# Kernel tuning notes

Hardware: AMD Instinct MI355X
Metric: run time of the kernel (lower is better)

The kernel has to match this reference:

```python
import jax, jax.numpy as jnp
import numpy as np

EPS = 1e-5


def ternarize(w):
    # TWN: delta = 0.7*mean|w|; alpha = mean of |w| over entries above delta
    delta = 0.7 * jnp.mean(jnp.abs(w))
    mask = (jnp.abs(w) > delta).astype(w.dtype)
    alpha = jnp.sum(jnp.abs(w) * mask) / jnp.maximum(jnp.sum(mask), 1.0)
    q = alpha * jnp.sign(w) * mask
    # straight-through estimator (matches torch `w + (q - w).detach()`)
    return w + jax.lax.stop_gradient(q - w)


def conv2d(x, w, stride, pad):
    # x: NCHW, w: OIHW
    return jax.lax.conv_general_dilated(
        x, w, window_strides=(stride, stride), padding=[(pad, pad), (pad, pad)],
        dimension_numbers=("NCHW", "OIHW", "NCHW"))


def batchnorm(x, gamma, beta, mean, var):
    # inference-mode BN over channel dim of NCHW
    inv = gamma / jnp.sqrt(var + EPS)
    return x * inv[None, :, None, None] + (beta - mean * inv)[None, :, None, None]


def setup_inputs() -> dict:
    key = jax.random.key(0)
    ks = jax.random.split(key, 12)
    d = {
        "x": jax.random.normal(ks[0], (64, 3, 224, 224), jnp.float32),
        "w1": jax.random.normal(ks[1], (32, 3, 3, 3), jnp.float32) * 0.1,
        "g1": jnp.ones((32,), jnp.float32), "b1": jnp.zeros((32,), jnp.float32),
        "m1": jax.random.normal(ks[2], (32,), jnp.float32) * 0.1,
        "v1": jax.random.uniform(ks[3], (32,), jnp.float32, 0.5, 1.5),
        "w2": jax.random.normal(ks[4], (64, 32, 3, 3), jnp.float32) * 0.05,
        "g2": jnp.ones((64,), jnp.float32), "b2": jnp.zeros((64,), jnp.float32),
        "m2": jax.random.normal(ks[5], (64,), jnp.float32) * 0.1,
        "v2": jax.random.uniform(ks[6], (64,), jnp.float32, 0.5, 1.5),
        "w3": jax.random.normal(ks[7], (128, 64, 3, 3), jnp.float32) * 0.05,
        "g3": jnp.ones((128,), jnp.float32), "b3": jnp.zeros((128,), jnp.float32),
        "m3": jax.random.normal(ks[8], (128,), jnp.float32) * 0.1,
        "v3": jax.random.uniform(ks[9], (128,), jnp.float32, 0.5, 1.5),
        "wl": jax.random.normal(ks[10], (10, 128), jnp.float32) * 0.1,
        "bl": jax.random.normal(ks[11], (10,), jnp.float32) * 0.01,
    }
    return d


def reference(x, w1, g1, b1, m1, v1, w2, g2, b2, m2, v2,
              w3, g3, b3, m3, v3, wl, bl):
    h = jax.nn.relu(batchnorm(conv2d(x, ternarize(w1), 2, 1), g1, b1, m1, v1))
    h = jax.nn.relu(batchnorm(conv2d(h, ternarize(w2), 1, 1), g2, b2, m2, v2))
    h = jax.nn.relu(batchnorm(conv2d(h, ternarize(w3), 2, 1), g3, b3, m3, v3))
    h = jnp.mean(h, axis=(2, 3))  # AdaptiveAvgPool2d((1,1)) + flatten -> [N,128]
    return h @ ternarize(wl).T + bl
```

## Files before the change

kernel.cpp:

```cpp
#include <hip/hip_runtime.h>
#include <cstddef>

typedef __attribute__((ext_vector_type(8))) short short8;
typedef __attribute__((ext_vector_type(4))) float floatx4;

__device__ __forceinline__ unsigned short f2bf(float f) {
  union { float f; unsigned u; } v; v.f = f;
  const unsigned r = v.u + 0x7fffu + ((v.u >> 16) & 1u);
  return (unsigned short)(r >> 16);
}

__device__ __forceinline__ float block_reduce_sum(float v, float* sm) {
#pragma unroll
  for (int off = 32; off > 0; off >>= 1) v += __shfl_down(v, off, 64);
  const int lane = threadIdx.x & 63, wid = threadIdx.x >> 6;
  __syncthreads();
  if (lane == 0) sm[wid] = v;
  __syncthreads();
  if (threadIdx.x == 0) {
    float t = 0.f;
    const int nw = (blockDim.x + 63) >> 6;
    for (int i = 0; i < nw; ++i) t += sm[i];
    sm[0] = t;
  }
  __syncthreads();
  return sm[0];
}

__device__ __forceinline__ void tsel(int t, const float* w0, const float* w1,
                                     const float* w2, const float* w3, int n0,
                                     int n1, int n2, int n3,
                                     const float*& w, int& n) {
  w = (t == 0) ? w0 : (t == 1) ? w1 : (t == 2) ? w2 : w3;
  n = (t == 0) ? n0 : (t == 1) ? n1 : (t == 2) ? n2 : n3;
}

__global__ __launch_bounds__(256) void tern_phase1(
    const float* w0, const float* w1, const float* w2, const float* w3,
    int n0, int n1, int n2, int n3, float* __restrict__ red) {
  __shared__ float sm[8];
  const float* w; int n;
  tsel(blockIdx.y, w0, w1, w2, w3, n0, n1, n2, n3, w, n);
  if ((int)blockIdx.x * 256 >= n) return;
  const int i = blockIdx.x * 256 + threadIdx.x;
  float s = (i < n) ? fabsf(w[i]) : 0.f;
  s = block_reduce_sum(s, sm);
  if (threadIdx.x == 0) atomicAdd(&red[blockIdx.y * 4 + 0], s);
}

__global__ __launch_bounds__(256) void tern_phase2(
    const float* w0, const float* w1, const float* w2, const float* w3,
    int n0, int n1, int n2, int n3, float* __restrict__ red) {
  __shared__ float sm[8];
  const float* w; int n;
  tsel(blockIdx.y, w0, w1, w2, w3, n0, n1, n2, n3, w, n);
  if ((int)blockIdx.x * 256 >= n) return;
  const float delta = 0.7f * red[blockIdx.y * 4 + 0] / (float)n;
  const int i = blockIdx.x * 256 + threadIdx.x;
  float c = 0.f, a = 0.f;
  if (i < n) {
    const float v = fabsf(w[i]);
    if (v > delta) { c = 1.f; a = v; }
  }
  c = block_reduce_sum(c, sm);
  a = block_reduce_sum(a, sm);
  if (threadIdx.x == 0) {
    atomicAdd(&red[blockIdx.y * 4 + 1], c);
    atomicAdd(&red[blockIdx.y * 4 + 2], a);
  }
}

__global__ __launch_bounds__(256) void prep_all(
    const float* w1, const float* w2, const float* w3, const float* wl,
    const float* g1, const float* b1, const float* m1, const float* v1,
    const float* g2, const float* b2, const float* m2, const float* v2,
    const float* g3, const float* b3, const float* m3, const float* v3,
    const float* __restrict__ red, float* q1t, float* ql,
    float* s1, float* bb1, float* s2, float* bb2, float* s3, float* bb3,
    unsigned short* bp2, unsigned short* bp3) {
  const int b = blockIdx.x, t = threadIdx.x;
  if (b == 0) {
    if (t < 32) {
      const float inv = g1[t] / sqrtf(v1[t] + 1e-5f);
      const float a = red[2] / fmaxf(red[1], 1.f);
      s1[t] = a * inv; bb1[t] = b1[t] - m1[t] * inv;
    } else if (t < 96) {
      const int c = t - 32;
      const float inv = g2[c] / sqrtf(v2[c] + 1e-5f);
      const float a = red[6] / fmaxf(red[5], 1.f);
      s2[c] = a * inv; bb2[c] = b2[c] - m2[c] * inv;
    } else if (t < 224) {
      const int c = t - 96;
      const float inv = g3[c] / sqrtf(v3[c] + 1e-5f);
      const float a = red[10] / fmaxf(red[9], 1.f);
      s3[c] = a * inv; bb3[c] = b3[c] - m3[c] * inv;
    }
  } else if (b <= 4) {
    const int idx = (b - 1) * 256 + t;
    if (idx < 864) {
      const float delta = 0.7f * red[0] / 864.f;
      const int tap = idx / 32, oc = idx % 32;
      const int ic = tap / 9, kh = (tap % 9) / 3, kw = tap % 3;
      const float v = w1[((oc * 3 + ic) * 3 + kh) * 3 + kw];
      q1t[idx] = (v > delta) ? 1.f : (v < -delta ? -1.f : 0.f);
    }
  } else if (b <= 9) {
    const int i = (b - 5) * 256 + t;
    if (i < 1280) {
      const float delta = 0.7f * red[12] / 1280.f;
      const float alpha = red[14] / fmaxf(red[13], 1.f);
      const float wi = wl[i];
      ql[i] = (fabsf(wi) > delta) ? copysignf(alpha, wi) : 0.f;
    }
  } else if (b <= 81) {
    const int idx = (b - 10) * 256 + t;
    const float delta = 0.7f * red[4] / 18432.f;
    const int k = idx / 64, n = idx % 64;
    const int tap = k / 32, ic = k % 32;
    const int kh = tap / 3, kw = tap % 3;
    const float v = w2[(((size_t)n * 32 + ic) * 3 + kh) * 3 + kw];
    bp2[((size_t)(k >> 3) * 64 + n) * 8 + (k & 7)] =
        (v > delta) ? 0x3F80u : (v < -delta ? 0xBF80u : 0u);
  } else {
    const int idx = (b - 82) * 256 + t;
    const float delta = 0.7f * red[8] / 73728.f;
    const int k = idx / 128, n = idx % 128;
    const int tap = k / 64, ic = k % 64;
    const int kh = tap / 3, kw = tap % 3;
    const float v = w3[(((size_t)n * 64 + ic) * 3 + kh) * 3 + kw];
    bp3[((size_t)(k >> 3) * 128 + n) * 8 + (k & 7)] =
        (v > delta) ? 0x3F80u : (v < -delta ? 0xBF80u : 0u);
  }
}

__global__ __launch_bounds__(256) void conv1_v2(
    const float* __restrict__ x, const float* __restrict__ q1t,
    const float* __restrict__ scale, const float* __restrict__ bias,
    unsigned short* __restrict__ y) {
  __shared__ float xs[15 * 225];
  const int n = blockIdx.y;
  const int oh0 = blockIdx.x * 2;
  const int t = threadIdx.x;
  const int ih_base = oh0 * 2 - 1;
  for (int idx = t; idx < 15 * 225; idx += 256) {
    const int row = idx / 225, s = idx % 225;
    const int ic = row / 5, dr = row % 5;
    const int ih = ih_base + dr, iw = s - 1;
    float v = 0.f;
    if ((unsigned)ih < 224u && (unsigned)iw < 224u)
      v = x[((size_t)n * 3 + ic) * 50176 + (size_t)ih * 224 + iw];
    xs[idx] = v;
  }
  __syncthreads();
  if (t >= 224) return;
  const int r = t / 112, ow = t % 112;
  float acc[32];
#pragma unroll
  for (int j = 0; j < 32; ++j) acc[j] = 0.f;
#pragma unroll
  for (int ic = 0; ic < 3; ++ic)
#pragma unroll
    for (int kh = 0; kh < 3; ++kh) {
      const float* xr = &xs[(ic * 5 + r * 2 + kh) * 225 + 2 * ow];
      const float xv0 = xr[0], xv1 = xr[1], xv2 = xr[2];
#pragma unroll
      for (int kw = 0; kw < 3; ++kw) {
        const float xv = (kw == 0) ? xv0 : (kw == 1) ? xv1 : xv2;
        const float* wrow = &q1t[(ic * 9 + kh * 3 + kw) * 32];
#pragma unroll
        for (int j = 0; j < 32; ++j) acc[j] += xv * wrow[j];
      }
    }
  const int oh = oh0 + r;
  unsigned pk[16];
#pragma unroll
  for (int h = 0; h < 16; ++h) {
    const float a0 = fmaxf(acc[2 * h] * scale[2 * h] + bias[2 * h], 0.f);
    const float a1 = fmaxf(acc[2 * h + 1] * scale[2 * h + 1] + bias[2 * h + 1], 0.f);
    pk[h] = (unsigned)f2bf(a0) | ((unsigned)f2bf(a1) << 16);
  }
  unsigned short* dst = y + (((size_t)n * 112 + oh) * 112 + ow) * 32;
#pragma unroll
  for (int v = 0; v < 4; ++v)
    *(uint4*)(dst + v * 8) = make_uint4(pk[4 * v], pk[4 * v + 1],
                                        pk[4 * v + 2], pk[4 * v + 3]);
}

__global__ __launch_bounds__(256) void conv2_halo(
    const unsigned short* __restrict__ xin,
    const unsigned short* __restrict__ bp,
    const float* __restrict__ scale, const float* __restrict__ bias,
    unsigned short* __restrict__ yout) {
  constexpr int PH = 10, PW = 18;
  __shared__ unsigned short patch[4 * PH * PW * 8];
  const int t = threadIdx.x;
  const int img = blockIdx.z;
  const int toh = blockIdx.x / 7, tow = blockIdx.x % 7;
  const int wave = t >> 6, lane = t & 63, quad = lane >> 4, l16 = lane & 15;
  const int oh0 = toh * 8, ow0 = tow * 16;

  for (int c = t; c < PH * PW * 4; c += 256) {
    const int pix = c >> 2, seg = c & 3;
    const int pi = pix / PW, pj = pix % PW;
    const int ih = oh0 - 1 + pi, iw = ow0 - 1 + pj;
    uint4 v = make_uint4(0u, 0u, 0u, 0u);
    if ((unsigned)ih < 112u && (unsigned)iw < 112u)
      v = *(const uint4*)(xin + (((size_t)img * 112 + ih) * 112 + iw) * 32 +
                          seg * 8);
    *(uint4*)(&patch[((seg * PH + pi) * PW + pj) * 8]) = v;
  }

  floatx4 acc[2][4];
#pragma unroll
  for (int mf = 0; mf < 2; ++mf)
#pragma unroll
    for (int nf = 0; nf < 4; ++nf) acc[mf][nf] = (floatx4){0.f, 0.f, 0.f, 0.f};

  short8 bcur[4], bnxt[4];
#pragma unroll
  for (int nf = 0; nf < 4; ++nf)
    bcur[nf] = *(const short8*)(bp + ((size_t)quad * 64 + nf * 16 + l16) * 8);
  __syncthreads();

#pragma unroll
  for (int tap = 0; tap < 9; ++tap) {
    const int kh = tap / 3, kw = tap % 3;
    if (tap + 1 < 9) {
      const int kg = (tap + 1) * 4 + quad;
#pragma unroll
      for (int nf = 0; nf < 4; ++nf)
        bnxt[nf] = *(const short8*)(bp + ((size_t)kg * 64 + nf * 16 + l16) * 8);
    }
#pragma unroll
    for (int mf = 0; mf < 2; ++mf) {
      const int pi = (wave * 2 + mf) + kh;
      const short8 a = *(const short8*)(
          &patch[((quad * PH + pi) * PW + l16 + kw) * 8]);
#pragma unroll
      for (int nf = 0; nf < 4; ++nf)
        acc[mf][nf] = __builtin_amdgcn_mfma_f32_16x16x32_bf16(
            a, bcur[nf], acc[mf][nf], 0, 0, 0);
    }
#pragma unroll
    for (int nf = 0; nf < 4; ++nf) bcur[nf] = bnxt[nf];
  }

  float sc[4], bs[4];
#pragma unroll
  for (int nf = 0; nf < 4; ++nf) {
    sc[nf] = scale[nf * 16 + l16];
    bs[nf] = bias[nf * 16 + l16];
  }
#pragma unroll
  for (int mf = 0; mf < 2; ++mf) {
    const int oh = oh0 + wave * 2 + mf;
#pragma unroll
    for (int r = 0; r < 4; ++r) {
      const int ow = ow0 + quad * 4 + r;
      const size_t base = (((size_t)img * 112 + oh) * 112 + ow) * 64;
#pragma unroll
      for (int nf = 0; nf < 4; ++nf) {
        const float vv = fmaxf(acc[mf][nf][r] * sc[nf] + bs[nf], 0.f);
        yout[base + nf * 16 + l16] = f2bf(vv);
      }
    }
  }
}

__global__ __launch_bounds__(256, 5) void conv3_pool(
    const unsigned short* __restrict__ act2,
    const unsigned short* __restrict__ bp3,
    const float* __restrict__ s3, const float* __restrict__ bb3,
    float* __restrict__ pooled) {
  __shared__ unsigned short c2p[4 * 17 * 18 * 8];
  __shared__ float pbuf[128];
  const int t = threadIdx.x;
  const int img = blockIdx.y;
  const int ty = blockIdx.x / 7, tx = blockIdx.x % 7;
  const int o3h0 = ty * 8, o3w0 = tx * 8;
  const int wave = t >> 6, lane = t & 63, quad = lane >> 4, l16 = lane & 15;

  int a3off[4];
#pragma unroll
  for (int mf = 0; mf < 4; ++mf) {
    const int px = mf * 16 + l16;
    a3off[mf] = ((quad * 17 + (px >> 3) * 2) * 18 + (px & 7)) * 8;
  }

  floatx4 acc3[4][2];
#pragma unroll
  for (int mf = 0; mf < 4; ++mf) {
    acc3[mf][0] = (floatx4){0.f, 0.f, 0.f, 0.f};
    acc3[mf][1] = (floatx4){0.f, 0.f, 0.f, 0.f};
  }

  const int h0 = o3h0 * 2 - 1, w0 = o3w0 * 2 - 1;
#pragma unroll
  for (int h = 0; h < 2; ++h) {
    if (h) __syncthreads();
    for (int c = t; c < 17 * 17 * 4; c += 256) {
      const int pix = c >> 2, seg = c & 3;
      const int pi = pix / 17, pj = pix % 17;
      const int ih = h0 + pi, iw = w0 + pj;
      uint4 v = make_uint4(0u, 0u, 0u, 0u);
      if ((unsigned)ih < 112u && (unsigned)iw < 112u)
        v = *(const uint4*)(act2 + (((size_t)img * 112 + ih) * 112 + iw) * 64 +
                            h * 32 + seg * 8);
      const int slot = (pj >> 1) + (pj & 1) * 9;
      *(uint4*)(&c2p[((seg * 17 + pi) * 18 + slot) * 8]) = v;
    }
    __syncthreads();
#pragma unroll
    for (int tap = 0; tap < 9; ++tap) {
      const int kh = tap / 3, kw = tap % 3;
      const int kg = tap * 8 + h * 4 + quad;
      const short8 b0 = *(const short8*)(
          bp3 + ((size_t)kg * 128 + wave * 32 + l16) * 8);
      const short8 b1 = *(const short8*)(
          bp3 + ((size_t)kg * 128 + wave * 32 + 16 + l16) * 8);
      const int toff = (kh * 18 + (kw >> 1) + (kw & 1) * 9) * 8;
#pragma unroll
      for (int mf = 0; mf < 4; ++mf) {
        const short8 a = *(const short8*)(&c2p[a3off[mf] + toff]);
        acc3[mf][0] = __builtin_amdgcn_mfma_f32_16x16x32_bf16(a, b0,
                                                              acc3[mf][0], 0, 0, 0);
        acc3[mf][1] = __builtin_amdgcn_mfma_f32_16x16x32_bf16(a, b1,
                                                              acc3[mf][1], 0, 0, 0);
      }
    }
  }

#pragma unroll
  for (int nf = 0; nf < 2; ++nf) {
    const int ch = wave * 32 + nf * 16 + l16;
    const float sc = s3[ch], bs = bb3[ch];
    float s = 0.f;
#pragma unroll
    for (int mf = 0; mf < 4; ++mf)
#pragma unroll
      for (int r = 0; r < 4; ++r)
        s += fmaxf(acc3[mf][nf][r] * sc + bs, 0.f);
    s += __shfl_xor(s, 16);
    s += __shfl_xor(s, 32);
    if (lane < 16) pbuf[ch] = s;
  }
  __syncthreads();
  if (t < 128) atomicAdd(&pooled[(size_t)img * 128 + t], pbuf[t]);
}

__global__ void linear_kernel(const float* __restrict__ pooled,
                              const float* __restrict__ ql,
                              const float* __restrict__ bl,
                              float* __restrict__ out) {
  const int idx = blockIdx.x * blockDim.x + threadIdx.x;
  if (idx >= 64 * 10) return;
  const int n = idx / 10, o = idx % 10;
  const float* p = pooled + (size_t)n * 128;
  const float* w = ql + (size_t)o * 128;
  float s = 0.f;
#pragma unroll 4
  for (int c = 0; c < 128; ++c) s += p[c] * w[c];
  out[idx] = s * (1.f / 3136.f) + bl[o];
}

extern "C" void kernel_launch(void* const* d_in, const int* in_sizes, int n_in,
                              void* d_out, int out_size, void* d_ws,
                              size_t ws_size, hipStream_t stream) {
  const float* x  = (const float*)d_in[0];
  const float* w1 = (const float*)d_in[1];
  const float* g1 = (const float*)d_in[2];
  const float* b1 = (const float*)d_in[3];
  const float* m1 = (const float*)d_in[4];
  const float* v1 = (const float*)d_in[5];
  const float* w2 = (const float*)d_in[6];
  const float* g2 = (const float*)d_in[7];
  const float* b2 = (const float*)d_in[8];
  const float* m2 = (const float*)d_in[9];
  const float* v2 = (const float*)d_in[10];
  const float* w3 = (const float*)d_in[11];
  const float* g3 = (const float*)d_in[12];
  const float* b3 = (const float*)d_in[13];
  const float* m3 = (const float*)d_in[14];
  const float* v3 = (const float*)d_in[15];
  const float* wl = (const float*)d_in[16];
  const float* bl = (const float*)d_in[17];
  float* out = (float*)d_out;

  float* Wf = (float*)d_ws;
  float* red = Wf;
  float* pooled = red + 16;
  float* q1t = pooled + 8192;
  float* ql = q1t + 864;
  float* s1 = ql + 1280;  float* bb1 = s1 + 32;
  float* s2 = bb1 + 32;   float* bb2 = s2 + 64;
  float* s3 = bb2 + 64;   float* bb3 = s3 + 128;
  unsigned short* Us = (unsigned short*)(bb3 + 128);
  unsigned short* bp2 = Us;
  unsigned short* bp3 = bp2 + 18432;
  unsigned short* act1 = bp3 + 73728;
  unsigned short* act2 = act1 + 25690112;

  hipMemsetAsync(red, 0, (16 + 8192) * sizeof(float), stream);
  tern_phase1<<<dim3(288, 4), 256, 0, stream>>>(w1, w2, w3, wl, 864, 18432,
                                                73728, 1280, red);
  tern_phase2<<<dim3(288, 4), 256, 0, stream>>>(w1, w2, w3, wl, 864, 18432,
                                                73728, 1280, red);
  prep_all<<<370, 256, 0, stream>>>(w1, w2, w3, wl, g1, b1, m1, v1, g2, b2,
                                    m2, v2, g3, b3, m3, v3, red, q1t, ql, s1,
                                    bb1, s2, bb2, s3, bb3, bp2, bp3);

  conv1_v2<<<dim3(56, 64), 256, 0, stream>>>(x, q1t, s1, bb1, act1);
  conv2_halo<<<dim3(98, 1, 64), 256, 0, stream>>>(act1, bp2, s2, bb2, act2);
  conv3_pool<<<dim3(49, 64), 256, 0, stream>>>(act2, bp3, s3, bb3, pooled);
  linear_kernel<<<3, 256, 0, stream>>>(pooled, ql, bl, out);
}
```

Before: 275.5 us.

## Fuse conv2 and conv3 into one kernel, recomputing conv2 halo tiles in LDS

Merges the conv2 and conv3+pool kernels. Each block computes a 17x17 conv2 output patch (with halo) from act1 in LDS and feeds it straight into conv3, so the large act2 tensor is never written to or read back from global memory. The weight layouts are rearranged to suit the new MFMA operand roles: weights become the A operand and pixels the B operand. The cost is redundant conv2 work on halo pixels (289 versus 256 per tile) and higher register and LDS pressure, which may reduce occupancy.

```diff
diff --git a/kernel.cpp b/kernel.cpp
--- a/kernel.cpp
+++ b/kernel.cpp
@@ -2,6 +2,7 @@
 #include <cstddef>
 
 typedef __attribute__((ext_vector_type(8))) short short8;
+typedef __attribute__((ext_vector_type(4))) short short4v;
 typedef __attribute__((ext_vector_type(4))) float floatx4;
 
 __device__ __forceinline__ unsigned short f2bf(float f) {
@@ -77,7 +78,7 @@
     const float* g3, const float* b3, const float* m3, const float* v3,
     const float* __restrict__ red, float* q1t, float* ql,
     float* s1, float* bb1, float* s2, float* bb2, float* s3, float* bb3,
-    unsigned short* bp2, unsigned short* bp3) {
+    unsigned short* w2t, unsigned short* w3t) {
   const int b = blockIdx.x, t = threadIdx.x;
   if (b == 0) {
     if (t < 32) {
@@ -115,21 +116,21 @@
   } else if (b <= 81) {
     const int idx = (b - 10) * 256 + t;
     const float delta = 0.7f * red[4] / 18432.f;
-    const int k = idx / 64, n = idx % 64;
-    const int tap = k / 32, ic = k % 32;
+    const int j = idx & 7, och2 = (idx >> 3) & 63;
+    const int quad = (idx >> 9) & 3, tap = idx >> 11;
+    const int ch1 = quad * 8 + j;
     const int kh = tap / 3, kw = tap % 3;
-    const float v = w2[(((size_t)n * 32 + ic) * 3 + kh) * 3 + kw];
-    bp2[((size_t)(k >> 3) * 64 + n) * 8 + (k & 7)] =
-        (v > delta) ? 0x3F80u : (v < -delta ? 0xBF80u : 0u);
+    const float v = w2[(((size_t)och2 * 32 + ch1) * 3 + kh) * 3 + kw];
+    w2t[idx] = (v > delta) ? 0x3F80u : (v < -delta ? 0xBF80u : 0u);
   } else {
     const int idx = (b - 82) * 256 + t;
     const float delta = 0.7f * red[8] / 73728.f;
-    const int k = idx / 128, n = idx % 128;
-    const int tap = k / 64, ic = k % 64;
+    const int j = idx & 7, och3 = (idx >> 3) & 127;
+    const int quad = (idx >> 10) & 3, h = (idx >> 12) & 1, tap = idx >> 13;
+    const int ch2 = h * 32 + quad * 8 + j;
     const int kh = tap / 3, kw = tap % 3;
-    const float v = w3[(((size_t)n * 64 + ic) * 3 + kh) * 3 + kw];
-    bp3[((size_t)(k >> 3) * 128 + n) * 8 + (k & 7)] =
-        (v > delta) ? 0x3F80u : (v < -delta ? 0xBF80u : 0u);
+    const float v = w3[(((size_t)och3 * 64 + ch2) * 3 + kh) * 3 + kw];
+    w3t[idx] = (v > delta) ? 0x3F80u : (v < -delta ? 0xBF80u : 0u);
   }
 }
 
@@ -186,93 +187,14 @@
                                         pk[4 * v + 2], pk[4 * v + 3]);
 }
 
-__global__ __launch_bounds__(256) void conv2_halo(
-    const unsigned short* __restrict__ xin,
-    const unsigned short* __restrict__ bp,
-    const float* __restrict__ scale, const float* __restrict__ bias,
-    unsigned short* __restrict__ yout) {
-  constexpr int PH = 10, PW = 18;
-  __shared__ unsigned short patch[4 * PH * PW * 8];
-  const int t = threadIdx.x;
-  const int img = blockIdx.z;
-  const int toh = blockIdx.x / 7, tow = blockIdx.x % 7;
-  const int wave = t >> 6, lane = t & 63, quad = lane >> 4, l16 = lane & 15;
-  const int oh0 = toh * 8, ow0 = tow * 16;
-
-  for (int c = t; c < PH * PW * 4; c += 256) {
-    const int pix = c >> 2, seg = c & 3;
-    const int pi = pix / PW, pj = pix % PW;
-    const int ih = oh0 - 1 + pi, iw = ow0 - 1 + pj;
-    uint4 v = make_uint4(0u, 0u, 0u, 0u);
-    if ((unsigned)ih < 112u && (unsigned)iw < 112u)
-      v = *(const uint4*)(xin + (((size_t)img * 112 + ih) * 112 + iw) * 32 +
-                          seg * 8);
-    *(uint4*)(&patch[((seg * PH + pi) * PW + pj) * 8]) = v;
-  }
-
-  floatx4 acc[2][4];
-#pragma unroll
-  for (int mf = 0; mf < 2; ++mf)
-#pragma unroll
-    for (int nf = 0; nf < 4; ++nf) acc[mf][nf] = (floatx4){0.f, 0.f, 0.f, 0.f};
-
-  short8 bcur[4], bnxt[4];
-#pragma unroll
-  for (int nf = 0; nf < 4; ++nf)
-    bcur[nf] = *(const short8*)(bp + ((size_t)quad * 64 + nf * 16 + l16) * 8);
-  __syncthreads();
-
-#pragma unroll
-  for (int tap = 0; tap < 9; ++tap) {
-    const int kh = tap / 3, kw = tap % 3;
-    if (tap + 1 < 9) {
-      const int kg = (tap + 1) * 4 + quad;
-#pragma unroll
-      for (int nf = 0; nf < 4; ++nf)
-        bnxt[nf] = *(const short8*)(bp + ((size_t)kg * 64 + nf * 16 + l16) * 8);
-    }
-#pragma unroll
-    for (int mf = 0; mf < 2; ++mf) {
-      const int pi = (wave * 2 + mf) + kh;
-      const short8 a = *(const short8*)(
-          &patch[((quad * PH + pi) * PW + l16 + kw) * 8]);
-#pragma unroll
-      for (int nf = 0; nf < 4; ++nf)
-        acc[mf][nf] = __builtin_amdgcn_mfma_f32_16x16x32_bf16(
-            a, bcur[nf], acc[mf][nf], 0, 0, 0);
-    }
-#pragma unroll
-    for (int nf = 0; nf < 4; ++nf) bcur[nf] = bnxt[nf];
-  }
-
-  float sc[4], bs[4];
-#pragma unroll
-  for (int nf = 0; nf < 4; ++nf) {
-    sc[nf] = scale[nf * 16 + l16];
-    bs[nf] = bias[nf * 16 + l16];
-  }
-#pragma unroll
-  for (int mf = 0; mf < 2; ++mf) {
-    const int oh = oh0 + wave * 2 + mf;
-#pragma unroll
-    for (int r = 0; r < 4; ++r) {
-      const int ow = ow0 + quad * 4 + r;
-      const size_t base = (((size_t)img * 112 + oh) * 112 + ow) * 64;
-#pragma unroll
-      for (int nf = 0; nf < 4; ++nf) {
-        const float vv = fmaxf(acc[mf][nf][r] * sc[nf] + bs[nf], 0.f);
-        yout[base + nf * 16 + l16] = f2bf(vv);
-      }
-    }
-  }
-}
-
-__global__ __launch_bounds__(256, 5) void conv3_pool(
-    const unsigned short* __restrict__ act2,
-    const unsigned short* __restrict__ bp3,
+__global__ __launch_bounds__(256) void conv23_fused(
+    const unsigned short* __restrict__ act1,
+    const unsigned short* __restrict__ w2t,
+    const unsigned short* __restrict__ w3t,
+    const float* __restrict__ s2, const float* __restrict__ bb2,
     const float* __restrict__ s3, const float* __restrict__ bb3,
     float* __restrict__ pooled) {
-  __shared__ unsigned short c2p[4 * 17 * 18 * 8];
+  __shared__ unsigned short lds[11552];
   __shared__ float pbuf[128];
   const int t = threadIdx.x;
   const int img = blockIdx.y;
@@ -280,69 +202,130 @@
   const int o3h0 = ty * 8, o3w0 = tx * 8;
   const int wave = t >> 6, lane = t & 63, quad = lane >> 4, l16 = lane & 15;
 
-  int a3off[4];
-#pragma unroll
-  for (int mf = 0; mf < 4; ++mf) {
-    const int px = mf * 16 + l16;
-    a3off[mf] = ((quad * 17 + (px >> 3) * 2) * 18 + (px & 7)) * 8;
-  }
-
-  floatx4 acc3[4][2];
-#pragma unroll
-  for (int mf = 0; mf < 4; ++mf) {
-    acc3[mf][0] = (floatx4){0.f, 0.f, 0.f, 0.f};
-    acc3[mf][1] = (floatx4){0.f, 0.f, 0.f, 0.f};
-  }
-
-  const int h0 = o3h0 * 2 - 1, w0 = o3w0 * 2 - 1;
-#pragma unroll
-  for (int h = 0; h < 2; ++h) {
-    if (h) __syncthreads();
-    for (int c = t; c < 17 * 17 * 4; c += 256) {
+  if (t < 128) pbuf[t] = 0.f;
+
+  {
+    const int h0 = o3h0 * 2 - 2, w0 = o3w0 * 2 - 2;
+    for (int c = t; c < 19 * 19 * 4; c += 256) {
       const int pix = c >> 2, seg = c & 3;
-      const int pi = pix / 17, pj = pix % 17;
+      const int pi = pix / 19, pj = pix % 19;
       const int ih = h0 + pi, iw = w0 + pj;
       uint4 v = make_uint4(0u, 0u, 0u, 0u);
       if ((unsigned)ih < 112u && (unsigned)iw < 112u)
-        v = *(const uint4*)(act2 + (((size_t)img * 112 + ih) * 112 + iw) * 64 +
-                            h * 32 + seg * 8);
-      const int slot = (pj >> 1) + (pj & 1) * 9;
-      *(uint4*)(&c2p[((seg * 17 + pi) * 18 + slot) * 8]) = v;
-    }
+        v = *(const uint4*)(act1 + (((size_t)img * 112 + ih) * 112 + iw) * 32 +
+                            seg * 8);
+      *(uint4*)(&lds[((seg * 19 + pi) * 19 + pj) * 8]) = v;
+    }
+  }
+
+  const int nfr = (wave == 3) ? 4 : 5;
+  int baddr[5], pxv[5], piw[5], pjw[5];
+#pragma unroll
+  for (int i = 0; i < 5; ++i) {
+    const int frag = wave + 4 * i;
+    const int px = frag * 16 + l16;
+    pxv[i] = px;
+    const int pc = (px < 289) ? px : 288;
+    piw[i] = pc / 17;
+    pjw[i] = pc % 17;
+    baddr[i] = ((quad * 19 + piw[i]) * 19 + pjw[i]) * 8;
+  }
+  const int p3i = wave * 2 + (l16 >> 3), p3j = l16 & 7;
+  const int b3base = ((p3i * 2) * 17 + p3j * 2) * 36 + quad * 8;
+
+  floatx4 acc2[5][4];
+#pragma unroll
+  for (int i = 0; i < 5; ++i)
+#pragma unroll
+    for (int f = 0; f < 4; ++f) acc2[i][f] = (floatx4){0.f, 0.f, 0.f, 0.f};
+  floatx4 acc3[8];
+#pragma unroll
+  for (int of = 0; of < 8; ++of) acc3[of] = (floatx4){0.f, 0.f, 0.f, 0.f};
+
+  __syncthreads();
+
+#pragma unroll
+  for (int tap = 0; tap < 9; ++tap) {
+    const int kh = tap / 3, kw = tap % 3;
+    short8 a[4];
+#pragma unroll
+    for (int f = 0; f < 4; ++f)
+      a[f] = *(const short8*)(w2t +
+          ((size_t)(tap * 4 + quad) * 64 + f * 16 + l16) * 8);
+    const int toff = (kh * 19 + kw) * 8;
+#pragma unroll
+    for (int i = 0; i < 5; ++i)
+      if (i < nfr) {
+        const short8 b = *(const short8*)(&lds[baddr[i] + toff]);
+#pragma unroll
+        for (int f = 0; f < 4; ++f)
+          acc2[i][f] = __builtin_amdgcn_mfma_f32_16x16x32_bf16(
+              a[f], b, acc2[i][f], 0, 0, 0);
+      }
+  }
+
+#pragma unroll
+  for (int h = 0; h < 2; ++h) {
+    __syncthreads();
+#pragma unroll
+    for (int i = 0; i < 5; ++i)
+      if (i < nfr && pxv[i] < 289) {
+        const bool zr = (o3h0 == 0 && piw[i] == 0) ||
+                        (o3w0 == 0 && pjw[i] == 0);
+#pragma unroll
+        for (int fl = 0; fl < 2; ++fl) {
+          const int f = 2 * h + fl;
+          const float4 sc = *(const float4*)&s2[f * 16 + quad * 4];
+          const float4 bs = *(const float4*)&bb2[f * 16 + quad * 4];
+          const float v0 = zr ? 0.f : fmaxf(acc2[i][f][0] * sc.x + bs.x, 0.f);
+          const float v1 = zr ? 0.f : fmaxf(acc2[i][f][1] * sc.y + bs.y, 0.f);
+          const float v2 = zr ? 0.f : fmaxf(acc2[i][f][2] * sc.z + bs.z, 0.f);
+          const float v3 = zr ? 0.f : fmaxf(acc2[i][f][3] * sc.w + bs.w, 0.f);
+          const unsigned u0 = (unsigned)f2bf(v0) | ((unsigned)f2bf(v1) << 16);
+          const unsigned u1 = (unsigned)f2bf(v2) | ((unsigned)f2bf(v3) << 16);
+          *(uint2*)(&lds[pxv[i] * 36 + fl * 16 + quad * 4]) =
+              make_uint2(u0, u1);
+        }
+      }
     __syncthreads();
 #pragma unroll
     for (int tap = 0; tap < 9; ++tap) {
       const int kh = tap / 3, kw = tap % 3;
-      const int kg = tap * 8 + h * 4 + quad;
-      const short8 b0 = *(const short8*)(
-          bp3 + ((size_t)kg * 128 + wave * 32 + l16) * 8);
-      const short8 b1 = *(const short8*)(
-          bp3 + ((size_t)kg * 128 + wave * 32 + 16 + l16) * 8);
-      const int toff = (kh * 18 + (kw >> 1) + (kw & 1) * 9) * 8;
-#pragma unroll
-      for (int mf = 0; mf < 4; ++mf) {
-        const short8 a = *(const short8*)(&c2p[a3off[mf] + toff]);
-        acc3[mf][0] = __builtin_amdgcn_mfma_f32_16x16x32_bf16(a, b0,
-                                                              acc3[mf][0], 0, 0, 0);
-        acc3[mf][1] = __builtin_amdgcn_mfma_f32_16x16x32_bf16(a, b1,
-                                                              acc3[mf][1], 0, 0, 0);
+      const int ba = b3base + (kh * 17 + kw) * 36;
+      const short4v lo = *(const short4v*)(&lds[ba]);
+      const short4v hi = *(const short4v*)(&lds[ba + 4]);
+      const short8 b = __builtin_shufflevector(lo, hi, 0, 1, 2, 3, 4, 5, 6, 7);
+#pragma unroll
+      for (int of = 0; of < 8; ++of) {
+        const short8 a = *(const short8*)(w3t +
+            ((size_t)((tap * 2 + h) * 4 + quad) * 128 + of * 16 + l16) * 8);
+        acc3[of] = __builtin_amdgcn_mfma_f32_16x16x32_bf16(
+            a, b, acc3[of], 0, 0, 0);
       }
     }
   }
 
 #pragma unroll
-  for (int nf = 0; nf < 2; ++nf) {
-    const int ch = wave * 32 + nf * 16 + l16;
-    const float sc = s3[ch], bs = bb3[ch];
-    float s = 0.f;
-#pragma unroll
-    for (int mf = 0; mf < 4; ++mf)
-#pragma unroll
-      for (int r = 0; r < 4; ++r)
-        s += fmaxf(acc3[mf][nf][r] * sc + bs, 0.f);
-    s += __shfl_xor(s, 16);
-    s += __shfl_xor(s, 32);
-    if (lane < 16) pbuf[ch] = s;
+  for (int of = 0; of < 8; ++of) {
+    const float4 sc = *(const float4*)&s3[of * 16 + quad * 4];
+    const float4 bs = *(const float4*)&bb3[of * 16 + quad * 4];
+    float v0 = fmaxf(acc3[of][0] * sc.x + bs.x, 0.f);
+    float v1 = fmaxf(acc3[of][1] * sc.y + bs.y, 0.f);
+    float v2 = fmaxf(acc3[of][2] * sc.z + bs.z, 0.f);
+    float v3 = fmaxf(acc3[of][3] * sc.w + bs.w, 0.f);
+#pragma unroll
+    for (int m = 1; m < 16; m <<= 1) {
+      v0 += __shfl_xor(v0, m);
+      v1 += __shfl_xor(v1, m);
+      v2 += __shfl_xor(v2, m);
+      v3 += __shfl_xor(v3, m);
+    }
+    if (l16 == 0) {
+      atomicAdd(&pbuf[of * 16 + quad * 4 + 0], v0);
+      atomicAdd(&pbuf[of * 16 + quad * 4 + 1], v1);
+      atomicAdd(&pbuf[of * 16 + quad * 4 + 2], v2);
+      atomicAdd(&pbuf[of * 16 + quad * 4 + 3], v3);
+    }
   }
   __syncthreads();
   if (t < 128) atomicAdd(&pooled[(size_t)img * 128 + t], pbuf[t]);
@@ -395,10 +378,9 @@
   float* s2 = bb1 + 32;   float* bb2 = s2 + 64;
   float* s3 = bb2 + 64;   float* bb3 = s3 + 128;
   unsigned short* Us = (unsigned short*)(bb3 + 128);
-  unsigned short* bp2 = Us;
-  unsigned short* bp3 = bp2 + 18432;
-  unsigned short* act1 = bp3 + 73728;
-  unsigned short* act2 = act1 + 25690112;
+  unsigned short* w2t = Us;
+  unsigned short* w3t = w2t + 18432;
+  unsigned short* act1 = w3t + 73728;
 
   hipMemsetAsync(red, 0, (16 + 8192) * sizeof(float), stream);
   tern_phase1<<<dim3(288, 4), 256, 0, stream>>>(w1, w2, w3, wl, 864, 18432,
@@ -407,10 +389,10 @@
                                                 73728, 1280, red);
   prep_all<<<370, 256, 0, stream>>>(w1, w2, w3, wl, g1, b1, m1, v1, g2, b2,
                                     m2, v2, g3, b3, m3, v3, red, q1t, ql, s1,
-                                    bb1, s2, bb2, s3, bb3, bp2, bp3);
+                                    bb1, s2, bb2, s3, bb3, w2t, w3t);
 
   conv1_v2<<<dim3(56, 64), 256, 0, stream>>>(x, q1t, s1, bb1, act1);
-  conv2_halo<<<dim3(98, 1, 64), 256, 0, stream>>>(act1, bp2, s2, bb2, act2);
-  conv3_pool<<<dim3(49, 64), 256, 0, stream>>>(act2, bp3, s3, bb3, pooled);
+  conv23_fused<<<dim3(49, 64), 256, 0, stream>>>(act1, w2t, w3t, s2, bb2, s3,
+                                                 bb3, pooled);
   linear_kernel<<<3, 256, 0, stream>>>(pooled, ql, bl, out);
 }
```

Result: slower. 313.6 us (+13.8%).

## Fold weight prep into phase2, compute BN scales in-kernel, persistent conv grids

Applied to the files above, without the earlier changes.

Removes the prep_all launch. Ternary weight packing moves into tern_phase2, which already knows delta, and each conv kernel now computes its BN scale and bias, plus the alpha factor, from the reduction buffer. conv2 and conv3 become grid-stride persistent kernels with 1568 blocks looping over tiles, and conv2 gets an occupancy hint of 6 blocks. This saves a launch and some prologue work, but the persistent loop adds extra syncs and may reduce latency hiding.

```diff
diff --git a/kernel.cpp b/kernel.cpp
--- a/kernel.cpp
+++ b/kernel.cpp
@@ -50,97 +50,64 @@
 
 __global__ __launch_bounds__(256) void tern_phase2(
     const float* w0, const float* w1, const float* w2, const float* w3,
-    int n0, int n1, int n2, int n3, float* __restrict__ red) {
+    int n0, int n1, int n2, int n3, float* __restrict__ red,
+    float* __restrict__ q1t, unsigned short* __restrict__ bp2,
+    unsigned short* __restrict__ bp3, float* __restrict__ ql) {
   __shared__ float sm[8];
   const float* w; int n;
-  tsel(blockIdx.y, w0, w1, w2, w3, n0, n1, n2, n3, w, n);
+  const int by = blockIdx.y;
+  tsel(by, w0, w1, w2, w3, n0, n1, n2, n3, w, n);
   if ((int)blockIdx.x * 256 >= n) return;
-  const float delta = 0.7f * red[blockIdx.y * 4 + 0] / (float)n;
+  const float delta = 0.7f * red[by * 4 + 0] / (float)n;
   const int i = blockIdx.x * 256 + threadIdx.x;
   float c = 0.f, a = 0.f;
+  float wv = 0.f;
   if (i < n) {
-    const float v = fabsf(w[i]);
-    if (v > delta) { c = 1.f; a = v; }
+    wv = w[i];
+    const float av = fabsf(wv);
+    if (av > delta) { c = 1.f; a = av; }
+  }
+  if (i < n) {
+    const float sgnf = (wv > delta) ? 1.f : (wv < -delta ? -1.f : 0.f);
+    const unsigned short sgnb =
+        (wv > delta) ? 0x3F80u : (wv < -delta ? 0xBF80u : 0u);
+    if (by == 0) {
+      q1t[(i % 27) * 32 + i / 27] = sgnf;
+    } else if (by == 1) {
+      const int k = (i % 9) * 32 + (i % 288) / 9;
+      bp2[((size_t)(k >> 3) * 64 + i / 288) * 8 + (k & 7)] = sgnb;
+    } else if (by == 2) {
+      const int k = (i % 9) * 64 + (i % 576) / 9;
+      bp3[((size_t)(k >> 3) * 128 + i / 576) * 8 + (k & 7)] = sgnb;
+    } else {
+      ql[i] = sgnf;
+    }
   }
   c = block_reduce_sum(c, sm);
   a = block_reduce_sum(a, sm);
   if (threadIdx.x == 0) {
-    atomicAdd(&red[blockIdx.y * 4 + 1], c);
-    atomicAdd(&red[blockIdx.y * 4 + 2], a);
-  }
-}
-
-__global__ __launch_bounds__(256) void prep_all(
-    const float* w1, const float* w2, const float* w3, const float* wl,
-    const float* g1, const float* b1, const float* m1, const float* v1,
-    const float* g2, const float* b2, const float* m2, const float* v2,
-    const float* g3, const float* b3, const float* m3, const float* v3,
-    const float* __restrict__ red, float* q1t, float* ql,
-    float* s1, float* bb1, float* s2, float* bb2, float* s3, float* bb3,
-    unsigned short* bp2, unsigned short* bp3) {
-  const int b = blockIdx.x, t = threadIdx.x;
-  if (b == 0) {
-    if (t < 32) {
-      const float inv = g1[t] / sqrtf(v1[t] + 1e-5f);
-      const float a = red[2] / fmaxf(red[1], 1.f);
-      s1[t] = a * inv; bb1[t] = b1[t] - m1[t] * inv;
-    } else if (t < 96) {
-      const int c = t - 32;
-      const float inv = g2[c] / sqrtf(v2[c] + 1e-5f);
-      const float a = red[6] / fmaxf(red[5], 1.f);
-      s2[c] = a * inv; bb2[c] = b2[c] - m2[c] * inv;
-    } else if (t < 224) {
-      const int c = t - 96;
-      const float inv = g3[c] / sqrtf(v3[c] + 1e-5f);
-      const float a = red[10] / fmaxf(red[9], 1.f);
-      s3[c] = a * inv; bb3[c] = b3[c] - m3[c] * inv;
-    }
-  } else if (b <= 4) {
-    const int idx = (b - 1) * 256 + t;
-    if (idx < 864) {
-      const float delta = 0.7f * red[0] / 864.f;
-      const int tap = idx / 32, oc = idx % 32;
-      const int ic = tap / 9, kh = (tap % 9) / 3, kw = tap % 3;
-      const float v = w1[((oc * 3 + ic) * 3 + kh) * 3 + kw];
-      q1t[idx] = (v > delta) ? 1.f : (v < -delta ? -1.f : 0.f);
-    }
-  } else if (b <= 9) {
-    const int i = (b - 5) * 256 + t;
-    if (i < 1280) {
-      const float delta = 0.7f * red[12] / 1280.f;
-      const float alpha = red[14] / fmaxf(red[13], 1.f);
-      const float wi = wl[i];
-      ql[i] = (fabsf(wi) > delta) ? copysignf(alpha, wi) : 0.f;
-    }
-  } else if (b <= 81) {
-    const int idx = (b - 10) * 256 + t;
-    const float delta = 0.7f * red[4] / 18432.f;
-    const int k = idx / 64, n = idx % 64;
-    const int tap = k / 32, ic = k % 32;
-    const int kh = tap / 3, kw = tap % 3;
-    const float v = w2[(((size_t)n * 32 + ic) * 3 + kh) * 3 + kw];
-    bp2[((size_t)(k >> 3) * 64 + n) * 8 + (k & 7)] =
-        (v > delta) ? 0x3F80u : (v < -delta ? 0xBF80u : 0u);
-  } else {
-    const int idx = (b - 82) * 256 + t;
-    const float delta = 0.7f * red[8] / 73728.f;
-    const int k = idx / 128, n = idx % 128;
-    const int tap = k / 64, ic = k % 64;
-    const int kh = tap / 3, kw = tap % 3;
-    const float v = w3[(((size_t)n * 64 + ic) * 3 + kh) * 3 + kw];
-    bp3[((size_t)(k >> 3) * 128 + n) * 8 + (k & 7)] =
-        (v > delta) ? 0x3F80u : (v < -delta ? 0xBF80u : 0u);
+    atomicAdd(&red[by * 4 + 1], c);
+    atomicAdd(&red[by * 4 + 2], a);
   }
 }
 
 __global__ __launch_bounds__(256) void conv1_v2(
     const float* __restrict__ x, const float* __restrict__ q1t,
-    const float* __restrict__ scale, const float* __restrict__ bias,
+    const float* __restrict__ red,
+    const float* __restrict__ g1, const float* __restrict__ b1,
+    const float* __restrict__ m1, const float* __restrict__ v1,
     unsigned short* __restrict__ y) {
   __shared__ float xs[15 * 225];
+  __shared__ float s1L[32], b1L[32];
   const int n = blockIdx.y;
   const int oh0 = blockIdx.x * 2;
   const int t = threadIdx.x;
+  if (t < 32) {
+    const float inv = g1[t] / sqrtf(v1[t] + 1e-5f);
+    const float a1 = red[2] / fmaxf(red[1], 1.f);
+    s1L[t] = a1 * inv;
+    b1L[t] = b1[t] - m1[t] * inv;
+  }
   const int ih_base = oh0 * 2 - 1;
   for (int idx = t; idx < 15 * 225; idx += 256) {
     const int row = idx / 225, s = idx % 225;
@@ -175,8 +142,8 @@
   unsigned pk[16];
 #pragma unroll
   for (int h = 0; h < 16; ++h) {
-    const float a0 = fmaxf(acc[2 * h] * scale[2 * h] + bias[2 * h], 0.f);
-    const float a1 = fmaxf(acc[2 * h + 1] * scale[2 * h + 1] + bias[2 * h + 1], 0.f);
+    const float a0 = fmaxf(acc[2 * h] * s1L[2 * h] + b1L[2 * h], 0.f);
+    const float a1 = fmaxf(acc[2 * h + 1] * s1L[2 * h + 1] + b1L[2 * h + 1], 0.f);
     pk[h] = (unsigned)f2bf(a0) | ((unsigned)f2bf(a1) << 16);
   }
   unsigned short* dst = y + (((size_t)n * 112 + oh) * 112 + ow) * 32;
@@ -186,82 +153,90 @@
                                         pk[4 * v + 2], pk[4 * v + 3]);
 }
 
-__global__ __launch_bounds__(256) void conv2_halo(
+__global__ __launch_bounds__(256, 6) void conv2_halo(
     const unsigned short* __restrict__ xin,
     const unsigned short* __restrict__ bp,
-    const float* __restrict__ scale, const float* __restrict__ bias,
+    const float* __restrict__ red,
+    const float* __restrict__ g2, const float* __restrict__ b2,
+    const float* __restrict__ m2, const float* __restrict__ v2,
     unsigned short* __restrict__ yout) {
   constexpr int PH = 10, PW = 18;
   __shared__ unsigned short patch[4 * PH * PW * 8];
   const int t = threadIdx.x;
-  const int img = blockIdx.z;
-  const int toh = blockIdx.x / 7, tow = blockIdx.x % 7;
   const int wave = t >> 6, lane = t & 63, quad = lane >> 4, l16 = lane & 15;
-  const int oh0 = toh * 8, ow0 = tow * 16;
-
-  for (int c = t; c < PH * PW * 4; c += 256) {
-    const int pix = c >> 2, seg = c & 3;
-    const int pi = pix / PW, pj = pix % PW;
-    const int ih = oh0 - 1 + pi, iw = ow0 - 1 + pj;
-    uint4 v = make_uint4(0u, 0u, 0u, 0u);
-    if ((unsigned)ih < 112u && (unsigned)iw < 112u)
-      v = *(const uint4*)(xin + (((size_t)img * 112 + ih) * 112 + iw) * 32 +
-                          seg * 8);
-    *(uint4*)(&patch[((seg * PH + pi) * PW + pj) * 8]) = v;
-  }
-
-  floatx4 acc[2][4];
-#pragma unroll
-  for (int mf = 0; mf < 2; ++mf)
-#pragma unroll
-    for (int nf = 0; nf < 4; ++nf) acc[mf][nf] = (floatx4){0.f, 0.f, 0.f, 0.f};
-
-  short8 bcur[4], bnxt[4];
-#pragma unroll
-  for (int nf = 0; nf < 4; ++nf)
-    bcur[nf] = *(const short8*)(bp + ((size_t)quad * 64 + nf * 16 + l16) * 8);
-  __syncthreads();
-
-#pragma unroll
-  for (int tap = 0; tap < 9; ++tap) {
-    const int kh = tap / 3, kw = tap % 3;
-    if (tap + 1 < 9) {
-      const int kg = (tap + 1) * 4 + quad;
-#pragma unroll
-      for (int nf = 0; nf < 4; ++nf)
-        bnxt[nf] = *(const short8*)(bp + ((size_t)kg * 64 + nf * 16 + l16) * 8);
-    }
+
+  float sc[4], bs[4];
+  const float a2 = red[6] / fmaxf(red[5], 1.f);
+#pragma unroll
+  for (int nf = 0; nf < 4; ++nf) {
+    const int ch = nf * 16 + l16;
+    const float inv = g2[ch] / sqrtf(v2[ch] + 1e-5f);
+    sc[nf] = a2 * inv;
+    bs[nf] = b2[ch] - m2[ch] * inv;
+  }
+
+  for (int tile = blockIdx.x; tile < 6272; tile += 1568) {
+    const int img = tile / 98, t2 = tile % 98;
+    const int oh0 = (t2 / 7) * 8, ow0 = (t2 % 7) * 16;
+    __syncthreads();
+    for (int c = t; c < PH * PW * 4; c += 256) {
+      const int pix = c >> 2, seg = c & 3;
+      const int pi = pix / PW, pj = pix % PW;
+      const int ih = oh0 - 1 + pi, iw = ow0 - 1 + pj;
+      uint4 v = make_uint4(0u, 0u, 0u, 0u);
+      if ((unsigned)ih < 112u && (unsigned)iw < 112u)
+        v = *(const uint4*)(xin + (((size_t)img * 112 + ih) * 112 + iw) * 32 +
+                            seg * 8);
+      *(uint4*)(&patch[((seg * PH + pi) * PW + pj) * 8]) = v;
+    }
+
+    floatx4 acc[2][4];
+#pragma unroll
+    for (int mf = 0; mf < 2; ++mf)
+#pragma unroll
+      for (int nf = 0; nf < 4; ++nf) acc[mf][nf] = (floatx4){0.f, 0.f, 0.f, 0.f};
+
+    short8 bcur[4], bnxt[4];
+#pragma unroll
+    for (int nf = 0; nf < 4; ++nf)
+      bcur[nf] = *(const short8*)(bp + ((size_t)quad * 64 + nf * 16 + l16) * 8);
+    __syncthreads();
+
+#pragma unroll
+    for (int tap = 0; tap < 9; ++tap) {
+      const int kh = tap / 3, kw = tap % 3;
+      if (tap + 1 < 9) {
+        const int kg = (tap + 1) * 4 + quad;
+#pragma unroll
+        for (int nf = 0; nf < 4; ++nf)
+          bnxt[nf] = *(const short8*)(bp + ((size_t)kg * 64 + nf * 16 + l16) * 8);
+      }
+#pragma unroll
+      for (int mf = 0; mf < 2; ++mf) {
+        const int pi = (wave * 2 + mf) + kh;
+        const short8 a = *(const short8*)(
+            &patch[((quad * PH + pi) * PW + l16 + kw) * 8]);
+#pragma unroll
+        for (int nf = 0; nf < 4; ++nf)
+          acc[mf][nf] = __builtin_amdgcn_mfma_f32_16x16x32_bf16(
+              a, bcur[nf], acc[mf][nf], 0, 0, 0);
+      }
+#pragma unroll
+      for (int nf = 0; nf < 4; ++nf) bcur[nf] = bnxt[nf];
+    }
+
 #pragma unroll
     for (int mf = 0; mf < 2; ++mf) {
-      const int pi = (wave * 2 + mf) + kh;
-      const short8 a = *(const short8*)(
-          &patch[((quad * PH + pi) * PW + l16 + kw) * 8]);
-#pragma unroll
-      for (int nf = 0; nf < 4; ++nf)
-        acc[mf][nf] = __builtin_amdgcn_mfma_f32_16x16x32_bf16(
-            a, bcur[nf], acc[mf][nf], 0, 0, 0);
-    }
-#pragma unroll
-    for (int nf = 0; nf < 4; ++nf) bcur[nf] = bnxt[nf];
-  }
-
-  float sc[4], bs[4];
-#pragma unroll
-  for (int nf = 0; nf < 4; ++nf) {
-    sc[nf] = scale[nf * 16 + l16];
-    bs[nf] = bias[nf * 16 + l16];
-  }
-#pragma unroll
-  for (int mf = 0; mf < 2; ++mf) {
-    const int oh = oh0 + wave * 2 + mf;
-#pragma unroll
-    for (int r = 0; r < 4; ++r) {
-      const int ow = ow0 + quad * 4 + r;
-      const size_t base = (((size_t)img * 112 + oh) * 112 + ow) * 64;
-#pragma unroll
-      for (int nf = 0; nf < 4; ++nf) {
-        const float vv = fmaxf(acc[mf][nf][r] * sc[nf] + bs[nf], 0.f);
-        yout[base + nf * 16 + l16] = f2bf(vv);
+      const int oh = oh0 + wave * 2 + mf;
+#pragma unroll
+      for (int r = 0; r < 4; ++r) {
+        const int ow = ow0 + quad * 4 + r;
+        const size_t base = (((size_t)img * 112 + oh) * 112 + ow) * 64;
+#pragma unroll
+        for (int nf = 0; nf < 4; ++nf) {
+          const float vv = fmaxf(acc[mf][nf][r] * sc[nf] + bs[nf], 0.f);
+          yout[base + nf * 16 + l16] = f2bf(vv);
+        }
       }
     }
   }
@@ -270,15 +245,24 @@
 __global__ __launch_bounds__(256, 5) void conv3_pool(
     const unsigned short* __restrict__ act2,
     const unsigned short* __restrict__ bp3,
-    const float* __restrict__ s3, const float* __restrict__ bb3,
+    const float* __restrict__ red,
+    const float* __restrict__ g3, const float* __restrict__ b3,
+    const float* __restrict__ m3, const float* __restrict__ v3,
     float* __restrict__ pooled) {
   __shared__ unsigned short c2p[4 * 17 * 18 * 8];
   __shared__ float pbuf[128];
   const int t = threadIdx.x;
-  const int img = blockIdx.y;
-  const int ty = blockIdx.x / 7, tx = blockIdx.x % 7;
-  const int o3h0 = ty * 8, o3w0 = tx * 8;
   const int wave = t >> 6, lane = t & 63, quad = lane >> 4, l16 = lane & 15;
+
+  float sc3[2], bs3[2];
+  const float a3 = red[10] / fmaxf(red[9], 1.f);
+#pragma unroll
+  for (int nf = 0; nf < 2; ++nf) {
+    const int ch = wave * 32 + nf * 16 + l16;
+    const float inv = g3[ch] / sqrtf(v3[ch] + 1e-5f);
+    sc3[nf] = a3 * inv;
+    bs3[nf] = b3[ch] - m3[ch] * inv;
+  }
 
   int a3off[4];
 #pragma unroll
@@ -287,70 +271,76 @@
     a3off[mf] = ((quad * 17 + (px >> 3) * 2) * 18 + (px & 7)) * 8;
   }
 
-  floatx4 acc3[4][2];
-#pragma unroll
-  for (int mf = 0; mf < 4; ++mf) {
-    acc3[mf][0] = (floatx4){0.f, 0.f, 0.f, 0.f};
-    acc3[mf][1] = (floatx4){0.f, 0.f, 0.f, 0.f};
-  }
-
-  const int h0 = o3h0 * 2 - 1, w0 = o3w0 * 2 - 1;
-#pragma unroll
-  for (int h = 0; h < 2; ++h) {
-    if (h) __syncthreads();
-    for (int c = t; c < 17 * 17 * 4; c += 256) {
-      const int pix = c >> 2, seg = c & 3;
-      const int pi = pix / 17, pj = pix % 17;
-      const int ih = h0 + pi, iw = w0 + pj;
-      uint4 v = make_uint4(0u, 0u, 0u, 0u);
-      if ((unsigned)ih < 112u && (unsigned)iw < 112u)
-        v = *(const uint4*)(act2 + (((size_t)img * 112 + ih) * 112 + iw) * 64 +
-                            h * 32 + seg * 8);
-      const int slot = (pj >> 1) + (pj & 1) * 9;
-      *(uint4*)(&c2p[((seg * 17 + pi) * 18 + slot) * 8]) = v;
+  for (int tile = blockIdx.x; tile < 3136; tile += 1568) {
+    const int img = tile / 49, tt = tile % 49;
+    const int o3h0 = (tt / 7) * 8, o3w0 = (tt % 7) * 8;
+    const int h0 = o3h0 * 2 - 1, w0 = o3w0 * 2 - 1;
+
+    floatx4 acc3[4][2];
+#pragma unroll
+    for (int mf = 0; mf < 4; ++mf) {
+      acc3[mf][0] = (floatx4){0.f, 0.f, 0.f, 0.f};
+      acc3[mf][1] = (floatx4){0.f, 0.f, 0.f, 0.f};
+    }
+
+#pragma unroll
+    for (int h = 0; h < 2; ++h) {
+      __syncthreads();
+      for (int c = t; c < 17 * 17 * 4; c += 256) {
+        const int pix = c >> 2, seg = c & 3;
+        const int pi = pix / 17, pj = pix % 17;
+        const int ih = h0 + pi, iw = w0 + pj;
+        uint4 v = make_uint4(0u, 0u, 0u, 0u);
+        if ((unsigned)ih < 112u && (unsigned)iw < 112u)
+          v = *(const uint4*)(act2 +
+                              (((size_t)img * 112 + ih) * 112 + iw) * 64 +
+                              h * 32 + seg * 8);
+        const int slot = (pj >> 1) + (pj & 1) * 9;
+        *(uint4*)(&c2p[((seg * 17 + pi) * 18 + slot) * 8]) = v;
+      }
+      __syncthreads();
+#pragma unroll
+      for (int tap = 0; tap < 9; ++tap) {
+        const int kh = tap / 3, kw = tap % 3;
+        const int kg = tap * 8 + h * 4 + quad;
+        const short8 b0 = *(const short8*)(
+            bp3 + ((size_t)kg * 128 + wave * 32 + l16) * 8);
+        const short8 b1 = *(const short8*)(
+            bp3 + ((size_t)kg * 128 + wave * 32 + 16 + l16) * 8);
+        const int toff = (kh * 18 + (kw >> 1) + (kw & 1) * 9) * 8;
+#pragma unroll
+        for (int mf = 0; mf < 4; ++mf) {
+          const short8 a = *(const short8*)(&c2p[a3off[mf] + toff]);
+          acc3[mf][0] = __builtin_amdgcn_mfma_f32_16x16x32_bf16(
+              a, b0, acc3[mf][0], 0, 0, 0);
+          acc3[mf][1] = __builtin_amdgcn_mfma_f32_16x16x32_bf16(
+              a, b1, acc3[mf][1], 0, 0, 0);
+        }
+      }
+    }
+
+#pragma unroll
+    for (int nf = 0; nf < 2; ++nf) {
+      const int ch = wave * 32 + nf * 16 + l16;
+      float s = 0.f;
+#pragma unroll
+      for (int mf = 0; mf < 4; ++mf)
+#pragma unroll
+        for (int r = 0; r < 4; ++r)
+          s += fmaxf(acc3[mf][nf][r] * sc3[nf] + bs3[nf], 0.f);
+      s += __shfl_xor(s, 16);
+      s += __shfl_xor(s, 32);
+      if (lane < 16) pbuf[ch] = s;
     }
     __syncthreads();
-#pragma unroll
-    for (int tap = 0; tap < 9; ++tap) {
-      const int kh = tap / 3, kw = tap % 3;
-      const int kg = tap * 8 + h * 4 + quad;
-      const short8 b0 = *(const short8*)(
-          bp3 + ((size_t)kg * 128 + wave * 32 + l16) * 8);
-      const short8 b1 = *(const short8*)(
-          bp3 + ((size_t)kg * 128 + wave * 32 + 16 + l16) * 8);
-      const int toff = (kh * 18 + (kw >> 1) + (kw & 1) * 9) * 8;
-#pragma unroll
-      for (int mf = 0; mf < 4; ++mf) {
-        const short8 a = *(const short8*)(&c2p[a3off[mf] + toff]);
-        acc3[mf][0] = __builtin_amdgcn_mfma_f32_16x16x32_bf16(a, b0,
-                                                              acc3[mf][0], 0, 0, 0);
-        acc3[mf][1] = __builtin_amdgcn_mfma_f32_16x16x32_bf16(a, b1,
-                                                              acc3[mf][1], 0, 0, 0);
-      }
-    }
-  }
-
-#pragma unroll
-  for (int nf = 0; nf < 2; ++nf) {
-    const int ch = wave * 32 + nf * 16 + l16;
-    const float sc = s3[ch], bs = bb3[ch];
-    float s = 0.f;
-#pragma unroll
-    for (int mf = 0; mf < 4; ++mf)
-#pragma unroll
-      for (int r = 0; r < 4; ++r)
-        s += fmaxf(acc3[mf][nf][r] * sc + bs, 0.f);
-    s += __shfl_xor(s, 16);
-    s += __shfl_xor(s, 32);
-    if (lane < 16) pbuf[ch] = s;
-  }
-  __syncthreads();
-  if (t < 128) atomicAdd(&pooled[(size_t)img * 128 + t], pbuf[t]);
+    if (t < 128) atomicAdd(&pooled[(size_t)img * 128 + t], pbuf[t]);
+  }
 }
 
 __global__ void linear_kernel(const float* __restrict__ pooled,
                               const float* __restrict__ ql,
                               const float* __restrict__ bl,
+                              const float* __restrict__ red,
                               float* __restrict__ out) {
   const int idx = blockIdx.x * blockDim.x + threadIdx.x;
   if (idx >= 64 * 10) return;
@@ -360,7 +350,8 @@
   float s = 0.f;
 #pragma unroll 4
   for (int c = 0; c < 128; ++c) s += p[c] * w[c];
-  out[idx] = s * (1.f / 3136.f) + bl[o];
+  const float alpha_l = red[14] / fmaxf(red[13], 1.f);
+  out[idx] = s * (alpha_l / 3136.f) + bl[o];
 }
 
 extern "C" void kernel_launch(void* const* d_in, const int* in_sizes, int n_in,
@@ -391,10 +382,7 @@
   float* pooled = red + 16;
   float* q1t = pooled + 8192;
   float* ql = q1t + 864;
-  float* s1 = ql + 1280;  float* bb1 = s1 + 32;
-  float* s2 = bb1 + 32;   float* bb2 = s2 + 64;
-  float* s3 = bb2 + 64;   float* bb3 = s3 + 128;
-  unsigned short* Us = (unsigned short*)(bb3 + 128);
+  unsigned short* Us = (unsigned short*)(ql + 1280);
   unsigned short* bp2 = Us;
   unsigned short* bp3 = bp2 + 18432;
   unsigned short* act1 = bp3 + 73728;
@@ -404,13 +392,13 @@
   tern_phase1<<<dim3(288, 4), 256, 0, stream>>>(w1, w2, w3, wl, 864, 18432,
                                                 73728, 1280, red);
   tern_phase2<<<dim3(288, 4), 256, 0, stream>>>(w1, w2, w3, wl, 864, 18432,
-                                                73728, 1280, red);
-  prep_all<<<370, 256, 0, stream>>>(w1, w2, w3, wl, g1, b1, m1, v1, g2, b2,
-                                    m2, v2, g3, b3, m3, v3, red, q1t, ql, s1,
-                                    bb1, s2, bb2, s3, bb3, bp2, bp3);
-
-  conv1_v2<<<dim3(56, 64), 256, 0, stream>>>(x, q1t, s1, bb1, act1);
-  conv2_halo<<<dim3(98, 1, 64), 256, 0, stream>>>(act1, bp2, s2, bb2, act2);
-  conv3_pool<<<dim3(49, 64), 256, 0, stream>>>(act2, bp3, s3, bb3, pooled);
-  linear_kernel<<<3, 256, 0, stream>>>(pooled, ql, bl, out);
-}
+                                                73728, 1280, red, q1t, bp2,
+                                                bp3, ql);
+
+  conv1_v2<<<dim3(56, 64), 256, 0, stream>>>(x, q1t, red, g1, b1, m1, v1,
+                                             act1);
+  conv2_halo<<<1568, 256, 0, stream>>>(act1, bp2, red, g2, b2, m2, v2, act2);
+  conv3_pool<<<1568, 256, 0, stream>>>(act2, bp3, red, g3, b3, m3, v3,
+                                       pooled);
+  linear_kernel<<<3, 256, 0, stream>>>(pooled, ql, bl, red, out);
+}
```

After: 792.1 us. 187% more time.
